# Performance work log

Measured on AMD Instinct MI355X. Metric: run time of the kernel, lower is better.

## Reference

```python
import jax, jax.numpy as jnp
import numpy as np

EPS = 1e-12  # F.normalize default eps (denominator = max(norm, eps))


def setup_inputs() -> dict:
    key = jax.random.key(0)
    ks = jax.random.split(key, 8)
    B, FIN, H, W = 4, 256, 64, 64
    N_MEM, SQ = 64, 16           # sqrt_fin = fin**0.5
    POS_CH = 2                    # PosEncoding concatenates one coord channel per dim
    CIN = FIN + POS_CH
    QK = N_MEM * SQ               # 1024
    # PosEncoding buffer: normalized coordinate grid in [-1, 1], shape [2, H, W]
    ys = jnp.linspace(-1.0, 1.0, H, dtype=jnp.float32)
    xs = jnp.linspace(-1.0, 1.0, W, dtype=jnp.float32)
    gy, gx = jnp.meshgrid(ys, xs, indexing='ij')
    pos = jnp.stack([gy, gx], axis=0)
    s = 0.02
    return {
        'x':    jax.random.normal(ks[0], (B, FIN, H, W), jnp.float32),
        'pos':  pos,
        'wq':   jax.random.normal(ks[1], (QK, CIN), jnp.float32) * s,
        'bq':   jnp.zeros((QK,), jnp.float32),
        'wk':   jax.random.normal(ks[2], (QK, CIN), jnp.float32) * s,
        'bk':   jnp.zeros((QK,), jnp.float32),
        'v':    jax.random.normal(ks[3], (N_MEM, FIN), jnp.float32) * s,
        'wout': jax.random.normal(ks[4], (FIN, FIN), jnp.float32) * s,
        'bout': jnp.zeros((FIN,), jnp.float32),
    }


def reference(x, pos, wq, bq, wk, bk, v, wout, bout):
    B, C, H, W = x.shape
    S = H * W
    n_mem, fin = v.shape
    sq = wq.shape[0] // n_mem
    # PosEncoding: concat coordinate channels
    posb = jnp.broadcast_to(pos[None], (B,) + pos.shape)
    xp = jnp.concatenate([x, posb], axis=1).reshape(B, C + pos.shape[0], S)
    # 1x1 conv projections (channel GEMMs)
    q = jnp.einsum('oc,bcs->bos', wq, xp) + bq[None, :, None]  # [B, n_mem*sq, S]
    k = jnp.einsum('oc,bcs->bos', wk, xp) + bk[None, :, None]
    q = q.reshape(B, n_mem, sq, S).transpose(0, 3, 1, 2)  # [B,S,m,sq]
    k = k.reshape(B, n_mem, sq, S).transpose(0, 3, 2, 1)  # [B,S,sq,m]
    # F.normalize: q over last dim (sqrt_fin), k over dim=1 (sqrt_fin)
    qn = q / jnp.maximum(jnp.linalg.norm(q, axis=-1, keepdims=True), EPS)
    kn = k / jnp.maximum(jnp.linalg.norm(k, axis=2, keepdims=True), EPS)
    # attn[b,s,m,n] = qn . kn ; dropout is identity in eval mode.
    # mean over memory slots m commutes with (attn @ v), so fuse:
    attn_mean = jnp.einsum('bsk,bskn->bsn', qn.mean(axis=2), kn)  # [B,S,n_mem]
    mem = attn_mean @ v                                            # [B,S,fin]
    mem = mem.transpose(0, 2, 1).reshape(B, fin, H, W)
    out = jnp.einsum('of,bfhw->bohw', wout, mem) + bout[None, :, None, None]
    return x + out
```

## Files before the change

### kernel.cpp

```cpp
#include <hip/hip_runtime.h>
#include <stdint.h>

#define EPSN 1e-12f

typedef float f32x16 __attribute__((ext_vector_type(16)));
typedef float f32x4 __attribute__((ext_vector_type(4)));
typedef __bf16 bf16x8 __attribute__((ext_vector_type(8)));

__device__ __forceinline__ unsigned short f2bf(float f) {
  union { float f; unsigned int u; } v; v.f = f;
  unsigned int u = v.u + 0x7FFFu + ((v.u >> 16) & 1u);
  return (unsigned short)(u >> 16);
}

__device__ __forceinline__ void dma16(const void* g, void* l) {
  __builtin_amdgcn_global_load_lds(
      (const __attribute__((address_space(1))) unsigned int*)g,
      (__attribute__((address_space(3))) unsigned int*)l, 16, 0, 0);
}

#define WQF_OFF 0
#define WKF_OFF (32 * 18 * 64 * 8)
#define WVP_OFF (2 * 32 * 18 * 64 * 8)

__global__ __launch_bounds__(256) void prep_kernel(
    const float* __restrict__ wq, const float* __restrict__ bq,
    const float* __restrict__ wk, const float* __restrict__ bk,
    const float* __restrict__ v, const float* __restrict__ wout,
    unsigned short* __restrict__ wsp) {
  int bid = blockIdx.x;
  if (bid < 512) {
    int isK = bid >= 256;
    int ob = (bid & 255) * 4;
    const float* w = isK ? wk : wq;
    const float* bb = isK ? bk : bq;
    unsigned short* dst = wsp + (isK ? WKF_OFF : WQF_OFF);
    for (int i = threadIdx.x; i < 4 * 129; i += 256) {
      int r = i / 129, q = i - r * 129;
      int o = ob + r, k = q * 2;
      float2 w2 = *(const float2*)(w + o * 258 + k);
      int g = o >> 5, col = o & 31;
      int ks = k >> 4, hi = (k >> 3) & 1, j = k & 7;
      uint32_t pk = (uint32_t)f2bf(w2.x) | ((uint32_t)f2bf(w2.y) << 16);
      *(uint32_t*)(dst + (((g * 18 + ks) * 64 + hi * 32 + col) << 3) + j) = pk;
    }
    for (int i = threadIdx.x; i < 4 * 30; i += 256) {
      int r = i / 30, kk = 258 + (i - r * 30);
      int o = ob + r;
      int g = o >> 5, col = o & 31;
      int ks = kk >> 4, hi = (kk >> 3) & 1, j = kk & 7;
      dst[(((g * 18 + ks) * 64 + hi * 32 + col) << 3) + j] =
          (kk == 258) ? f2bf(bb[o]) : (unsigned short)0;
    }
  } else {
    int idx = (bid - 512) * 256 + threadIdx.x;
    int fc = idx & 15, m = (idx >> 4) & 63, o = idx >> 10;
    const f32x4* wo = (const f32x4*)(wout + o * 256 + fc * 16);
    const f32x4* vm = (const f32x4*)(v + m * 256 + fc * 16);
    float s = 0.f;
#pragma unroll
    for (int f = 0; f < 4; ++f) {
      f32x4 a = wo[f], bvv = vm[f];
      s += a[0]*bvv[0] + a[1]*bvv[1] + a[2]*bvv[2] + a[3]*bvv[3];
    }
    s += __shfl_xor(s, 1, 64);
    s += __shfl_xor(s, 2, 64);
    s += __shfl_xor(s, 4, 64);
    s += __shfl_xor(s, 8, 64);
    if (fc == 0) wsp[WVP_OFF + o * 64 + m] = f2bf(s);
  }
}

#define KP 296
#define QS 66
#define AT 72

__global__ __launch_bounds__(1024, 4) void fused_kernel(
    const float* __restrict__ x, const float* __restrict__ pos,
    const unsigned short* __restrict__ wsp, const float* __restrict__ bout,
    float* __restrict__ out) {
  __shared__ __align__(16) unsigned short aBuf[3 * 32 * 512];
  __shared__ __align__(16) unsigned short xp[64 * KP];
  __shared__ __align__(16) float qbarL[16 * QS];
  __shared__ __align__(16) unsigned short attnM[64 * AT];
  __shared__ float boutL[256];

  const int tid = threadIdx.x;
  const int lane = tid & 63;
  const int wid = __builtin_amdgcn_readfirstlane(tid >> 6);
  const int px = lane & 31, q2 = lane >> 5;
  const int P0 = blockIdx.x * 64;
  const int b = P0 >> 12, s0 = P0 & 4095;

#define ISSUE(wb, ks_) do {                                              \
    int _sl = (ks_) % 3;                                                 \
    dma16(wb + ((2 * wid) * 18 + (ks_)) * 512 + lane * 8,                \
          &aBuf[_sl * 16384 + (2 * wid) * 512]);                         \
    dma16(wb + ((2 * wid + 1) * 18 + (ks_)) * 512 + lane * 8,            \
          &aBuf[_sl * 16384 + (2 * wid + 1) * 512]);                     \
  } while (0)

  ISSUE((wsp + WQF_OFF), 0);
  ISSUE((wsp + WQF_OFF), 1);

  uint32_t* xp32 = (uint32_t*)xp;
  for (int i = tid; i < 64 * 152; i += 1024) {
    int dc = i & 7, pp = (i >> 3) & 63, dh = i >> 9;
    int dcol = dh * 8 + dc;
    if (dcol < 148) {
      int c0 = dcol * 2;
      float v0, v1;
      if (c0 < 256) {
        v0 = x[(b * 256 + c0) * 4096 + s0 + pp];
        v1 = x[(b * 256 + c0 + 1) * 4096 + s0 + pp];
      } else if (c0 == 256) {
        v0 = pos[s0 + pp];
        v1 = pos[4096 + s0 + pp];
      } else {
        v0 = (c0 == 258) ? 1.0f : 0.0f;
        v1 = 0.0f;
      }
      xp32[pp * 148 + dcol] = (uint32_t)f2bf(v0) | ((uint32_t)f2bf(v1) << 16);
    }
  }
  if (tid < 256) boutL[tid] = bout[tid];
  for (int i = tid; i < 16 * QS; i += 1024) qbarL[i] = 0.f;
  __syncthreads();

#define COMPUTEA(ks_, b0_, b1_) do {                                     \
    int _sl = (ks_) % 3;                                                 \
    bf16x8 _a0 = *(const bf16x8*)&aBuf[_sl * 16384 + (2 * wid) * 512 + lane * 8];     \
    bf16x8 _a1 = *(const bf16x8*)&aBuf[_sl * 16384 + (2 * wid + 1) * 512 + lane * 8]; \
    acc00 = __builtin_amdgcn_mfma_f32_32x32x16_bf16(_a0, b0_, acc00, 0, 0, 0); \
    acc01 = __builtin_amdgcn_mfma_f32_32x32x16_bf16(_a0, b1_, acc01, 0, 0, 0); \
    acc10 = __builtin_amdgcn_mfma_f32_32x32x16_bf16(_a1, b0_, acc10, 0, 0, 0); \
    acc11 = __builtin_amdgcn_mfma_f32_32x32x16_bf16(_a1, b1_, acc11, 0, 0, 0); \
  } while (0)

#define PHASE(wb) do {                                                   \
    _Pragma("unroll 4")                                                  \
    for (int ks = 0; ks < 16; ++ks) {                                    \
      bf16x8 _b0 = *(const bf16x8*)&xp[px * KP + ks * 16 + q2 * 8];      \
      bf16x8 _b1 = *(const bf16x8*)&xp[(32 + px) * KP + ks * 16 + q2 * 8]; \
      ISSUE(wb, ks + 2);                                                 \
      asm volatile("s_waitcnt vmcnt(4)" ::: "memory");                   \
      COMPUTEA(ks, _b0, _b1);                                            \
    }                                                                    \
    {                                                                    \
      bf16x8 _b0 = *(const bf16x8*)&xp[px * KP + 16 * 16 + q2 * 8];      \
      bf16x8 _b1 = *(const bf16x8*)&xp[(32 + px) * KP + 16 * 16 + q2 * 8]; \
      asm volatile("s_waitcnt vmcnt(2)" ::: "memory");                   \
      COMPUTEA(16, _b0, _b1);                                            \
    }                                                                    \
    {                                                                    \
      bf16x8 _b0 = *(const bf16x8*)&xp[px * KP + 17 * 16 + q2 * 8];      \
      bf16x8 _b1 = *(const bf16x8*)&xp[(32 + px) * KP + 17 * 16 + q2 * 8]; \
      asm volatile("s_waitcnt vmcnt(0)" ::: "memory");                   \
      COMPUTEA(17, _b0, _b1);                                            \
    }                                                                    \
  } while (0)

  f32x16 acc00 = (f32x16)0.f, acc01 = (f32x16)0.f,
         acc10 = (f32x16)0.f, acc11 = (f32x16)0.f;
  PHASE((wsp + WQF_OFF));

  ISSUE((wsp + WKF_OFF), 0);
  ISSUE((wsp + WKF_OFF), 1);

  {
    float qsum[2][8];
#pragma unroll
    for (int nt = 0; nt < 2; ++nt)
#pragma unroll
      for (int r = 0; r < 8; ++r) qsum[nt][r] = 0.f;
#pragma unroll
    for (int ot = 0; ot < 2; ++ot) {
#pragma unroll
      for (int nt = 0; nt < 2; ++nt) {
        const f32x16 a = ot ? (nt ? acc11 : acc10) : (nt ? acc01 : acc00);
        float s20 = 0.f, s21 = 0.f;
#pragma unroll
        for (int r = 0; r < 8; ++r) {
          s20 = fmaf(a[r], a[r], s20);
          s21 = fmaf(a[r + 8], a[r + 8], s21);
        }
        s20 += __shfl_xor(s20, 32, 64);
        s21 += __shfl_xor(s21, 32, 64);
        float i0 = 1.0f / fmaxf(sqrtf(s20), EPSN);
        float i1 = 1.0f / fmaxf(sqrtf(s21), EPSN);
#pragma unroll
        for (int r = 0; r < 8; ++r) qsum[nt][r] += a[r] * i0 + a[r + 8] * i1;
      }
    }
#pragma unroll
    for (int nt = 0; nt < 2; ++nt)
#pragma unroll
      for (int r = 0; r < 8; ++r) {
        int j = (r & 3) + ((r >> 2) << 3) + (q2 << 2);
        atomicAdd(&qbarL[j * QS + nt * 32 + px], qsum[nt][r] * (1.0f / 64.0f));
      }
  }
  __syncthreads();

  acc00 = (f32x16)0.f; acc01 = (f32x16)0.f;
  acc10 = (f32x16)0.f; acc11 = (f32x16)0.f;
  PHASE((wsp + WKF_OFF));

  {
    float qb[2][8];
#pragma unroll
    for (int nt = 0; nt < 2; ++nt)
#pragma unroll
      for (int r = 0; r < 8; ++r) {
        int j = (r & 3) + ((r >> 2) << 3) + (q2 << 2);
        qb[nt][r] = qbarL[j * QS + nt * 32 + px];
      }
#pragma unroll
    for (int ot = 0; ot < 2; ++ot) {
#pragma unroll
      for (int nt = 0; nt < 2; ++nt) {
        const f32x16 a = ot ? (nt ? acc11 : acc10) : (nt ? acc01 : acc00);
        float s20 = 0.f, s21 = 0.f, sp0 = 0.f, sp1 = 0.f;
#pragma unroll
        for (int r = 0; r < 8; ++r) {
          s20 = fmaf(a[r], a[r], s20);         sp0 = fmaf(qb[nt][r], a[r], sp0);
          s21 = fmaf(a[r + 8], a[r + 8], s21); sp1 = fmaf(qb[nt][r], a[r + 8], sp1);
        }
        s20 += __shfl_xor(s20, 32, 64);
        s21 += __shfl_xor(s21, 32, 64);
        sp0 += __shfl_xor(sp0, 32, 64);
        sp1 += __shfl_xor(sp1, 32, 64);
        if (q2 == 0) {
          int m0 = wid * 4 + ot * 2;
          attnM[(nt * 32 + px) * AT + m0]     = f2bf(sp0 / fmaxf(sqrtf(s20), EPSN));
          attnM[(nt * 32 + px) * AT + m0 + 1] = f2bf(sp1 / fmaxf(sqrtf(s21), EPSN));
        }
      }
    }
  }
  __syncthreads();

  {
    const int otile = wid >> 1, pxt = wid & 1;
    f32x16 e = (f32x16)0.f;
    const unsigned short* wv = wsp + WVP_OFF + (otile * 32 + px) * 64 + q2 * 8;
    const unsigned short* ab = &attnM[(pxt * 32 + px) * AT + q2 * 8];
#pragma unroll
    for (int ks = 0; ks < 4; ++ks) {
      bf16x8 av = *(const bf16x8*)(wv + ks * 16);
      bf16x8 bv = *(const bf16x8*)(ab + ks * 16);
      e = __builtin_amdgcn_mfma_f32_32x32x16_bf16(av, bv, e, 0, 0, 0);
    }
#pragma unroll
    for (int r = 0; r < 16; ++r) {
      const int o = otile * 32 + (r & 3) + ((r >> 2) << 3) + (q2 << 2);
      const int p = pxt * 32 + px;
      const int gi = (b * 256 + o) * 4096 + s0 + p;
      out[gi] = x[gi] + boutL[o] + e[r];
    }
  }
#undef PHASE
#undef COMPUTEA
#undef ISSUE
}

extern "C" void kernel_launch(void* const* d_in, const int* in_sizes, int n_in,
                              void* d_out, int out_size, void* d_ws, size_t ws_size,
                              hipStream_t stream) {
  const float* x    = (const float*)d_in[0];
  const float* pos  = (const float*)d_in[1];
  const float* wq   = (const float*)d_in[2];
  const float* bq   = (const float*)d_in[3];
  const float* wk   = (const float*)d_in[4];
  const float* bk   = (const float*)d_in[5];
  const float* v    = (const float*)d_in[6];
  const float* wout = (const float*)d_in[7];
  const float* bout = (const float*)d_in[8];
  float* out = (float*)d_out;
  unsigned short* wsp = (unsigned short*)d_ws;

  hipLaunchKernelGGL(prep_kernel, dim3(1536), dim3(256), 0, stream,
                     wq, bq, wk, bk, v, wout, wsp);
  hipLaunchKernelGGL(fused_kernel, dim3(256), dim3(1024), 0, stream,
                     x, pos, wsp, bout, out);
}
```

Measured before the change: 131.1 us.

## Load weight fragments directly to registers and trim padded K steps

Drops the LDS triple-buffered global_load_lds staging of weight tiles and has each wave read its own A fragments straight from global memory into registers, prefetching one K-step ahead. It also shrinks the padded reduction depth from 18 to 17 k-steps, cutting one MFMA step per phase, and restructures the x staging so each thread issues eight independent loads before converting. This removes LDS traffic and waitcnt stalls and frees shared memory, at the cost of more global or L2 latency exposure, since the prefetch is only one step deep.

```diff
diff --git a/kernel.cpp b/kernel.cpp
--- a/kernel.cpp
+++ b/kernel.cpp
@@ -13,15 +13,10 @@
   return (unsigned short)(u >> 16);
 }
 
-__device__ __forceinline__ void dma16(const void* g, void* l) {
-  __builtin_amdgcn_global_load_lds(
-      (const __attribute__((address_space(1))) unsigned int*)g,
-      (__attribute__((address_space(3))) unsigned int*)l, 16, 0, 0);
-}
-
+#define NKS 17
 #define WQF_OFF 0
-#define WKF_OFF (32 * 18 * 64 * 8)
-#define WVP_OFF (2 * 32 * 18 * 64 * 8)
+#define WKF_OFF (32 * NKS * 64 * 8)
+#define WVP_OFF (2 * 32 * NKS * 64 * 8)
 
 __global__ __launch_bounds__(256) void prep_kernel(
     const float* __restrict__ wq, const float* __restrict__ bq,
@@ -42,14 +37,14 @@
       int g = o >> 5, col = o & 31;
       int ks = k >> 4, hi = (k >> 3) & 1, j = k & 7;
       uint32_t pk = (uint32_t)f2bf(w2.x) | ((uint32_t)f2bf(w2.y) << 16);
-      *(uint32_t*)(dst + (((g * 18 + ks) * 64 + hi * 32 + col) << 3) + j) = pk;
-    }
-    for (int i = threadIdx.x; i < 4 * 30; i += 256) {
-      int r = i / 30, kk = 258 + (i - r * 30);
+      *(uint32_t*)(dst + (((g * NKS + ks) * 64 + hi * 32 + col) << 3) + j) = pk;
+    }
+    for (int i = threadIdx.x; i < 4 * 14; i += 256) {
+      int r = i / 14, kk = 258 + (i - r * 14);
       int o = ob + r;
       int g = o >> 5, col = o & 31;
       int ks = kk >> 4, hi = (kk >> 3) & 1, j = kk & 7;
-      dst[(((g * 18 + ks) * 64 + hi * 32 + col) << 3) + j] =
+      dst[(((g * NKS + ks) * 64 + hi * 32 + col) << 3) + j] =
           (kk == 258) ? f2bf(bb[o]) : (unsigned short)0;
     }
   } else {
@@ -79,7 +74,6 @@
     const float* __restrict__ x, const float* __restrict__ pos,
     const unsigned short* __restrict__ wsp, const float* __restrict__ bout,
     float* __restrict__ out) {
-  __shared__ __align__(16) unsigned short aBuf[3 * 32 * 512];
   __shared__ __align__(16) unsigned short xp[64 * KP];
   __shared__ __align__(16) float qbarL[16 * QS];
   __shared__ __align__(16) unsigned short attnM[64 * AT];
@@ -92,80 +86,68 @@
   const int P0 = blockIdx.x * 64;
   const int b = P0 >> 12, s0 = P0 & 4095;
 
-#define ISSUE(wb, ks_) do {                                              \
-    int _sl = (ks_) % 3;                                                 \
-    dma16(wb + ((2 * wid) * 18 + (ks_)) * 512 + lane * 8,                \
-          &aBuf[_sl * 16384 + (2 * wid) * 512]);                         \
-    dma16(wb + ((2 * wid + 1) * 18 + (ks_)) * 512 + lane * 8,            \
-          &aBuf[_sl * 16384 + (2 * wid + 1) * 512]);                     \
-  } while (0)
-
-  ISSUE((wsp + WQF_OFF), 0);
-  ISSUE((wsp + WQF_OFF), 1);
+  const int wtoff = (2 * wid) * NKS * 512 + lane * 8;
+  const unsigned short* wqf = wsp + WQF_OFF + wtoff;
+  const unsigned short* wkf = wsp + WKF_OFF + wtoff;
+
+  bf16x8 A0 = *(const bf16x8*)(wqf);
+  bf16x8 A1 = *(const bf16x8*)(wqf + NKS * 512);
 
   uint32_t* xp32 = (uint32_t*)xp;
-  for (int i = tid; i < 64 * 152; i += 1024) {
-    int dc = i & 7, pp = (i >> 3) & 63, dh = i >> 9;
-    int dcol = dh * 8 + dc;
-    if (dcol < 148) {
-      int c0 = dcol * 2;
-      float v0, v1;
-      if (c0 < 256) {
-        v0 = x[(b * 256 + c0) * 4096 + s0 + pp];
-        v1 = x[(b * 256 + c0 + 1) * 4096 + s0 + pp];
-      } else if (c0 == 256) {
-        v0 = pos[s0 + pp];
-        v1 = pos[4096 + s0 + pp];
-      } else {
-        v0 = (c0 == 258) ? 1.0f : 0.0f;
-        v1 = 0.0f;
-      }
-      xp32[pp * 148 + dcol] = (uint32_t)f2bf(v0) | ((uint32_t)f2bf(v1) << 16);
+  {
+    const float* xrow = x + b * 256 * 4096 + s0;
+    float v0[8], v1[8];
+#pragma unroll
+    for (int it = 0; it < 8; ++it) {
+      int item = tid + it * 1024;
+      int pp = item & 63, dcol = item >> 6;
+      v0[it] = xrow[(2 * dcol) * 4096 + pp];
+      v1[it] = xrow[(2 * dcol + 1) * 4096 + pp];
+    }
+#pragma unroll
+    for (int it = 0; it < 8; ++it) {
+      int item = tid + it * 1024;
+      int pp = item & 63, dcol = item >> 6;
+      xp32[pp * 148 + dcol] =
+          (uint32_t)f2bf(v0[it]) | ((uint32_t)f2bf(v1[it]) << 16);
+    }
+    if (tid < 512) {
+      int pp = tid & 63, dcol = 128 + (tid >> 6);
+      float t0 = 0.f, t1 = 0.f;
+      if (dcol == 128) { t0 = pos[s0 + pp]; t1 = pos[4096 + s0 + pp]; }
+      else if (dcol == 129) { t0 = 1.0f; }
+      xp32[pp * 148 + dcol] = (uint32_t)f2bf(t0) | ((uint32_t)f2bf(t1) << 16);
     }
   }
   if (tid < 256) boutL[tid] = bout[tid];
   for (int i = tid; i < 16 * QS; i += 1024) qbarL[i] = 0.f;
   __syncthreads();
 
-#define COMPUTEA(ks_, b0_, b1_) do {                                     \
-    int _sl = (ks_) % 3;                                                 \
-    bf16x8 _a0 = *(const bf16x8*)&aBuf[_sl * 16384 + (2 * wid) * 512 + lane * 8];     \
-    bf16x8 _a1 = *(const bf16x8*)&aBuf[_sl * 16384 + (2 * wid + 1) * 512 + lane * 8]; \
-    acc00 = __builtin_amdgcn_mfma_f32_32x32x16_bf16(_a0, b0_, acc00, 0, 0, 0); \
-    acc01 = __builtin_amdgcn_mfma_f32_32x32x16_bf16(_a0, b1_, acc01, 0, 0, 0); \
-    acc10 = __builtin_amdgcn_mfma_f32_32x32x16_bf16(_a1, b0_, acc10, 0, 0, 0); \
-    acc11 = __builtin_amdgcn_mfma_f32_32x32x16_bf16(_a1, b1_, acc11, 0, 0, 0); \
-  } while (0)
-
-#define PHASE(wb) do {                                                   \
-    _Pragma("unroll 4")                                                  \
-    for (int ks = 0; ks < 16; ++ks) {                                    \
-      bf16x8 _b0 = *(const bf16x8*)&xp[px * KP + ks * 16 + q2 * 8];      \
-      bf16x8 _b1 = *(const bf16x8*)&xp[(32 + px) * KP + ks * 16 + q2 * 8]; \
-      ISSUE(wb, ks + 2);                                                 \
-      asm volatile("s_waitcnt vmcnt(4)" ::: "memory");                   \
-      COMPUTEA(ks, _b0, _b1);                                            \
-    }                                                                    \
-    {                                                                    \
-      bf16x8 _b0 = *(const bf16x8*)&xp[px * KP + 16 * 16 + q2 * 8];      \
-      bf16x8 _b1 = *(const bf16x8*)&xp[(32 + px) * KP + 16 * 16 + q2 * 8]; \
-      asm volatile("s_waitcnt vmcnt(2)" ::: "memory");                   \
-      COMPUTEA(16, _b0, _b1);                                            \
-    }                                                                    \
-    {                                                                    \
-      bf16x8 _b0 = *(const bf16x8*)&xp[px * KP + 17 * 16 + q2 * 8];      \
-      bf16x8 _b1 = *(const bf16x8*)&xp[(32 + px) * KP + 17 * 16 + q2 * 8]; \
-      asm volatile("s_waitcnt vmcnt(0)" ::: "memory");                   \
-      COMPUTEA(17, _b0, _b1);                                            \
-    }                                                                    \
+#define PHASE(WB, AI0, AI1) do {                                          \
+    bf16x8 _A0 = (AI0), _A1 = (AI1);                                      \
+    _Pragma("unroll")                                                     \
+    for (int ks = 0; ks < NKS; ++ks) {                                    \
+      bf16x8 _N0 = _A0, _N1 = _A1;                                        \
+      if (ks + 1 < NKS) {                                                 \
+        _N0 = *(const bf16x8*)((WB) + (ks + 1) * 512);                    \
+        _N1 = *(const bf16x8*)((WB) + NKS * 512 + (ks + 1) * 512);        \
+      }                                                                   \
+      bf16x8 _b0 = *(const bf16x8*)&xp[px * KP + ks * 16 + q2 * 8];       \
+      bf16x8 _b1 = *(const bf16x8*)&xp[(32 + px) * KP + ks * 16 + q2 * 8];\
+      acc00 = __builtin_amdgcn_mfma_f32_32x32x16_bf16(_A0, _b0, acc00, 0, 0, 0); \
+      acc01 = __builtin_amdgcn_mfma_f32_32x32x16_bf16(_A0, _b1, acc01, 0, 0, 0); \
+      acc10 = __builtin_amdgcn_mfma_f32_32x32x16_bf16(_A1, _b0, acc10, 0, 0, 0); \
+      acc11 = __builtin_amdgcn_mfma_f32_32x32x16_bf16(_A1, _b1, acc11, 0, 0, 0); \
+      _A0 = _N0; _A1 = _N1;                                               \
+    }                                                                     \
   } while (0)
 
   f32x16 acc00 = (f32x16)0.f, acc01 = (f32x16)0.f,
          acc10 = (f32x16)0.f, acc11 = (f32x16)0.f;
-  PHASE((wsp + WQF_OFF));
-
-  ISSUE((wsp + WKF_OFF), 0);
-  ISSUE((wsp + WKF_OFF), 1);
+  PHASE(wqf, A0, A1);
+
+  bf16x8 K0 = *(const bf16x8*)(wkf);
+  bf16x8 K1 = *(const bf16x8*)(wkf + NKS * 512);
 
   {
     float qsum[2][8];
@@ -204,7 +186,7 @@
 
   acc00 = (f32x16)0.f; acc01 = (f32x16)0.f;
   acc10 = (f32x16)0.f; acc11 = (f32x16)0.f;
-  PHASE((wsp + WKF_OFF));
+  PHASE(wkf, K0, K1);
 
   {
     float qb[2][8];
@@ -260,8 +242,6 @@
     }
   }
 #undef PHASE
-#undef COMPUTEA
-#undef ISSUE
 }
 
 extern "C" void kernel_launch(void* const* d_in, const int* in_sizes, int n_in,
```

Result: slower. 134.4 us (+2.6%).
